# Kernel optimization log

Measured on AMD Instinct MI355X. Metric: run time of the kernel, lower is better.

## Reference

```python
import jax, jax.numpy as jnp
import numpy as np
from jax import lax

H = 12  # num_heads

def conv1d_same(x, w, b):
    # x: [B, Cin, L], w: [Cout, Cin, K] (torch Conv1d layout), 'same' padding
    y = lax.conv_general_dilated(x, w, window_strides=(1,), padding='SAME',
                                 dimension_numbers=('NCH', 'OIH', 'NCH'))
    return y + b[None, :, None]

def setup_inputs() -> dict:
    key = jax.random.key(0)
    ks = jax.random.split(key, 16)
    B, N, C = 8, 4096, 768
    d = C // H
    s = 0.02
    return {
        'x': jax.random.normal(ks[0], (B, N, C), dtype=jnp.float32),
        'qkv_w': jax.random.normal(ks[1], (3 * C, C), dtype=jnp.float32) * s,
        'proj_w': jax.random.normal(ks[2], (C, C), dtype=jnp.float32) * s,
        'proj_b': jnp.zeros((C,), dtype=jnp.float32),
        'conv_w': jax.random.normal(ks[3], (d, d, 5), dtype=jnp.float32) * s,  # k=5 from log2(768)
        'conv_b': jnp.zeros((d,), dtype=jnp.float32),
        'fc_w': jax.random.normal(ks[4], (d, d), dtype=jnp.float32) * s,
        'fc_b': jnp.zeros((d,), dtype=jnp.float32),
        'dw1_w': jax.random.normal(ks[5], (d, d, 3), dtype=jnp.float32) * s,
        'dw1_b': jnp.zeros((d,), dtype=jnp.float32),
        'dw2_w': jax.random.normal(ks[6], (d, d, 5), dtype=jnp.float32) * s,
        'dw2_b': jnp.zeros((d,), dtype=jnp.float32),
    }

def reference(x, qkv_w, proj_w, proj_b, conv_w, conv_b, fc_w, fc_b, dw1_w, dw1_b, dw2_w, dw2_b):
    B, N, C = x.shape
    d = C // H
    scale = d ** (-0.5)
    # qkv projection -> [3, B, H, N, d]
    qkv = (x @ qkv_w.T).reshape(B, N, 3, H, d).transpose(2, 0, 3, 1, 4)
    q, k, v = qkv[0], qkv[1], qkv[2]
    # SE-style gate: global avg over tokens, conv over channel axis, sigmoid
    res = jnp.mean(v, axis=2).reshape(B * H, d, 1)          # [BH, d, 1]
    res = conv1d_same(res, conv_w, conv_b)                   # [BH, d, 1]
    res = jax.nn.sigmoid(res).transpose(0, 2, 1).reshape(B, H, 1, d)
    # value branch: two 1D convs over token axis (channels = head_dim)
    vch = v.reshape(B * H, N, d).transpose(0, 2, 1)          # [BH, d, N]
    v2 = conv1d_same(vch, dw1_w, dw1_b) + conv1d_same(vch, dw2_w, dw2_b)
    v2 = v2.transpose(0, 2, 1).reshape(B, H, N, d)
    # channel attention: (scaled k)^T @ q -> [B, H, d, d]
    kq = jnp.einsum('bhnd,bhne->bhde', k * scale, q)
    a = jax.nn.relu(kq) @ fc_w.T + fc_b
    a = jax.nn.softmax(a + kq, axis=-1)
    # (a @ v2^T)^T -> [B, H, N, d]
    out = jnp.einsum('bhde,bhne->bhnd', a, v2)
    out = res * out
    out = out.transpose(0, 2, 1, 3).reshape(B, N, C)
    return out @ proj_w.T + proj_b
```

## Files before the change

kernel.cpp:

```cpp
#include <hip/hip_runtime.h>
#include <hip/hip_bf16.h>
#include <cstdint>
#include <cstddef>

typedef unsigned short u16;
typedef __attribute__((ext_vector_type(4))) unsigned short u16x4;
typedef __attribute__((ext_vector_type(8))) unsigned short u16x8;
typedef __attribute__((ext_vector_type(8))) short bf16x8;
typedef __attribute__((ext_vector_type(4))) float f32x4;

#define BB 8
#define NN 4096
#define CC 768
#define HH 12
#define DD 64
#define NHEADS 96
#define QKVSZ 25165824LL

__device__ inline float b2f(u16 u) { return __uint_as_float(((unsigned)u) << 16); }
__device__ inline u16 f2b(float f) {
    unsigned u = __float_as_uint(f);
    return (u16)((u + 0x7fffu + ((u >> 16) & 1u)) >> 16);
}
__device__ inline f32x4 zero4() { f32x4 z = {0.f, 0.f, 0.f, 0.f}; return z; }

__device__ __forceinline__ void gl_lds16(const u16* g, u16* l) {
    __builtin_amdgcn_global_load_lds(
        (const __attribute__((address_space(1))) void*)g,
        (__attribute__((address_space(3))) void*)l, 16, 0, 0);
}

__global__ void cast_all(const float* __restrict__ x, const float* __restrict__ w1,
                         const float* __restrict__ w2, u16* __restrict__ xb,
                         u16* __restrict__ wqkv, u16* __restrict__ wproj) {
    const long n0 = 25165824, n1 = 1769472, n2 = 589824;
    long i0 = (long)(blockIdx.x * blockDim.x + threadIdx.x) * 4;
    long stride = (long)gridDim.x * blockDim.x * 4;
    for (long j = i0; j < n0 + n1 + n2; j += stride) {
        const float* s; u16* d; long k;
        if (j < n0)            { s = x;  d = xb;    k = j; }
        else if (j < n0 + n1)  { s = w1; d = wqkv;  k = j - n0; }
        else                   { s = w2; d = wproj; k = j - n0 - n1; }
        float4 v = *(const float4*)(s + k);
        u16x4 o;
        o[0] = f2b(v.x); o[1] = f2b(v.y); o[2] = f2b(v.z); o[3] = f2b(v.w);
        *(u16x4*)(d + k) = o;
    }
}

template <int MODE>
__global__ __launch_bounds__(256) void gemm128e(const u16* __restrict__ A, const u16* __restrict__ Bm,
                                                const float* __restrict__ bias, void* __restrict__ out,
                                                int ncol) {
    constexpr int K = 768;
    constexpr int NT = K / 32;
    __shared__ __align__(16) u16 lA[2][128 * 32];
    __shared__ __align__(16) u16 lB[2][128 * 32];
    const int tid = threadIdx.x;
    const int lane = tid & 63, wid = tid >> 6;
    const int wr = wid >> 1, wc = wid & 1;
    const int li = lane & 15, g = lane >> 4;

    const int nwg = gridDim.x, chunk = nwg >> 3;
    const int swz = ((int)blockIdx.x & 7) * chunk + ((int)blockIdx.x >> 3);
    const int col0 = (swz % ncol) * 128;
    const int row0 = (swz / ncol) * 128;

    const int srow = lane >> 2;
    const int scol = ((lane & 3) ^ ((lane >> 3) & 3)) * 8;

    f32x4 acc[4][4];
#pragma unroll
    for (int i = 0; i < 4; ++i)
#pragma unroll
        for (int j = 0; j < 4; ++j) acc[i][j] = zero4();

    const int r0s = wid * 32;

    gl_lds16(A  + (size_t)(row0 + r0s +      srow) * K + scol, &lA[0][ r0s       * 32]);
    gl_lds16(A  + (size_t)(row0 + r0s + 16 + srow) * K + scol, &lA[0][(r0s + 16) * 32]);
    gl_lds16(Bm + (size_t)(col0 + r0s +      srow) * K + scol, &lB[0][ r0s       * 32]);
    gl_lds16(Bm + (size_t)(col0 + r0s + 16 + srow) * K + scol, &lB[0][(r0s + 16) * 32]);

    int buf = 0;
    for (int t = 0; t < NT; ++t) {
        __syncthreads();
        if (t + 1 < NT) {
            const int kt = (t + 1) * 32;
            const int nb = buf ^ 1;
            gl_lds16(A  + (size_t)(row0 + r0s +      srow) * K + kt + scol, &lA[nb][ r0s       * 32]);
            gl_lds16(A  + (size_t)(row0 + r0s + 16 + srow) * K + kt + scol, &lA[nb][(r0s + 16) * 32]);
            gl_lds16(Bm + (size_t)(col0 + r0s +      srow) * K + kt + scol, &lB[nb][ r0s       * 32]);
            gl_lds16(Bm + (size_t)(col0 + r0s + 16 + srow) * K + kt + scol, &lB[nb][(r0s + 16) * 32]);
        }
        bf16x8 af[4], bf_[4];
#pragma unroll
        for (int i = 0; i < 4; ++i) {
            int ra = wr * 64 + i * 16 + li;
            af[i] = *(const bf16x8*)((const char*)&lA[buf][0] +
                                     ra * 64 + ((g ^ ((ra >> 1) & 3)) << 4));
            int rb = wc * 64 + i * 16 + li;
            bf_[i] = *(const bf16x8*)((const char*)&lB[buf][0] +
                                      rb * 64 + ((g ^ ((rb >> 1) & 3)) << 4));
        }
#pragma unroll
        for (int i = 0; i < 4; ++i)
#pragma unroll
            for (int j = 0; j < 4; ++j)
                acc[i][j] = __builtin_amdgcn_mfma_f32_16x16x32_bf16(af[i], bf_[j], acc[i][j], 0, 0, 0);
        buf ^= 1;
    }

#pragma unroll
    for (int i = 0; i < 4; ++i) {
#pragma unroll
        for (int j = 0; j < 4; ++j) {
            int c = col0 + wc * 64 + j * 16 + li;
            if constexpr (MODE == 0) {
                int part = c / 768, rem = c % 768;
                int h = rem >> 6, dd = rem & 63;
#pragma unroll
                for (int e = 0; e < 4; ++e) {
                    int r = row0 + wr * 64 + i * 16 + g * 4 + e;
                    int b = r >> 12, n = r & 4095;
                    ((u16*)out)[(((size_t)part * NHEADS + b * HH + h) * NN + n) * DD + dd] =
                        f2b(acc[i][j][e]);
                }
            } else {
                float bb = bias[c];
#pragma unroll
                for (int e = 0; e < 4; ++e) {
                    int r = row0 + wr * 64 + i * 16 + g * 4 + e;
                    ((float*)out)[(size_t)r * 768 + c] = acc[i][j][e] + bb;
                }
            }
        }
    }
}

__global__ __launch_bounds__(256) void kq_mean(const u16* __restrict__ qkv, float* __restrict__ kqp,
                                               float* __restrict__ meanp) {
    const int head = blockIdx.x, part = blockIdx.y;
    const int tid = threadIdx.x, lane = tid & 63, wid = tid >> 6;
    __shared__ __align__(16) u16 tiles[4][2][32 * 64];
    __shared__ float sred[16 * 64];

    if (part == 4) {
        const u16* vh = qkv + 2 * QKVSZ + (size_t)head * NN * DD;
        int rg = tid >> 4, cg = tid & 15;
        float s0 = 0.f, s1 = 0.f, s2 = 0.f, s3 = 0.f;
        for (int it = 0; it < 256; ++it) {
            int n = rg + it * 16;
            u16x4 v = *(const u16x4*)(vh + (size_t)n * DD + cg * 4);
            s0 += b2f(v[0]); s1 += b2f(v[1]); s2 += b2f(v[2]); s3 += b2f(v[3]);
        }
        sred[rg * 64 + cg * 4 + 0] = s0;
        sred[rg * 64 + cg * 4 + 1] = s1;
        sred[rg * 64 + cg * 4 + 2] = s2;
        sred[rg * 64 + cg * 4 + 3] = s3;
        __syncthreads();
        if (tid < 64) {
            float s = 0.f;
#pragma unroll
            for (int rg2 = 0; rg2 < 16; ++rg2) s += sred[rg2 * 64 + tid];
            meanp[head * 64 + tid] = s;
        }
        return;
    }

    u16* kt = tiles[wid][0];
    u16* qt = tiles[wid][1];
    const u16* qh = qkv + (size_t)head * NN * DD;
    const u16* kh = qkv + QKVSZ + (size_t)head * NN * DD;
    const int nbase = part * 1024 + wid * 256;

    f32x4 acc[4][4];
#pragma unroll
    for (int i = 0; i < 4; ++i)
#pragma unroll
        for (int j = 0; j < 4; ++j) acc[i][j] = zero4();

    const int srow = lane >> 3, schunk = (lane & 7) * 8;
    const int g8 = (lane >> 4) * 8, li = lane & 15;

    for (int it = 0; it < 8; ++it) {
        int n0 = nbase + it * 32;
#pragma unroll
        for (int p = 0; p < 4; ++p) {
            int r = srow + p * 8;
            *(u16x8*)(kt + r * 64 + schunk) = *(const u16x8*)(kh + (size_t)(n0 + r) * DD + schunk);
            *(u16x8*)(qt + r * 64 + schunk) = *(const u16x8*)(qh + (size_t)(n0 + r) * DD + schunk);
        }
        bf16x8 af[4], bf_[4];
#pragma unroll
        for (int i = 0; i < 4; ++i)
#pragma unroll
            for (int j = 0; j < 8; ++j) af[i][j] = (short)kt[(g8 + j) * 64 + i * 16 + li];
#pragma unroll
        for (int i = 0; i < 4; ++i)
#pragma unroll
            for (int j = 0; j < 8; ++j) bf_[i][j] = (short)qt[(g8 + j) * 64 + i * 16 + li];
#pragma unroll
        for (int i = 0; i < 4; ++i)
#pragma unroll
            for (int j = 0; j < 4; ++j)
                acc[i][j] = __builtin_amdgcn_mfma_f32_16x16x32_bf16(af[i], bf_[j], acc[i][j], 0, 0, 0);
    }

    const int slot = part * 4 + wid;
    const int g = lane >> 4;
    float* dst = kqp + ((size_t)head * 16 + slot) * 4096;
#pragma unroll
    for (int i = 0; i < 4; ++i)
#pragma unroll
        for (int j = 0; j < 4; ++j)
#pragma unroll
            for (int e = 0; e < 4; ++e)
                dst[(i * 16 + g * 4 + e) * 64 + j * 16 + li] = acc[i][j][e];
}

__global__ __launch_bounds__(256) void head_finish(
    const float* __restrict__ kqp, const float* __restrict__ meanp,
    const float* __restrict__ conv_w, const float* __restrict__ conv_b,
    const float* __restrict__ fc_w, const float* __restrict__ fc_b,
    const float* __restrict__ dw1_w, const float* __restrict__ dw1_b,
    const float* __restrict__ dw2_w, const float* __restrict__ dw2_b,
    u16* __restrict__ eff, float* __restrict__ effb) {
    const int head = blockIdx.x;
    const int tid = threadIdx.x;
    __shared__ float skq[64 * 64];
    __shared__ float sa[64 * 64];
    __shared__ float sgate[64];
    __shared__ float sw2[64 * 16 * 5];
    __shared__ float sw1[64 * 16 * 3];

    for (int idx = tid; idx < 4096; idx += 256) {
        float s = 0.f;
#pragma unroll
        for (int p = 0; p < 16; ++p) s += kqp[((size_t)head * 16 + p) * 4096 + idx];
        skq[idx] = s * 0.125f;
    }
    __syncthreads();
    if (tid < 64) {
        float gsum = conv_b[tid];
        for (int i = 0; i < 64; ++i)
            gsum += conv_w[(tid * 64 + i) * 5 + 2] * (meanp[head * 64 + i] * (1.f / 4096.f));
        sgate[tid] = 1.f / (1.f + __expf(-gsum));
    }

    {
        int rr = tid >> 2, cg = (tid & 3) * 16;
        for (int c = cg; c < cg + 16; ++c) {
            float s = fc_b[c];
            for (int e = 0; e < 64; ++e) s += fmaxf(skq[rr * 64 + e], 0.f) * fc_w[c * 64 + e];
            sa[rr * 64 + c] = s + skq[rr * 64 + c];
        }
    }
    __syncthreads();
    if (tid < 64) {
        float m = -1e30f;
        for (int e = 0; e < 64; ++e) m = fmaxf(m, sa[tid * 64 + e]);
        float s = 0.f;
        for (int e = 0; e < 64; ++e) {
            float p = __expf(sa[tid * 64 + e] - m);
            sa[tid * 64 + e] = p;
            s += p;
        }
        float inv = 1.f / s;
        for (int e = 0; e < 64; ++e) sa[tid * 64 + e] *= inv;
    }
    __syncthreads();
    if (tid < 64) {
        float s = 0.f;
        for (int e = 0; e < 64; ++e) s += sa[tid * 64 + e] * (dw1_b[e] + dw2_b[e]);
        effb[head * 64 + tid] = sgate[tid] * s;
    }

    for (int ig = 0; ig < 4; ++ig) {
        __syncthreads();
        for (int idx = tid; idx < 64 * 16 * 5; idx += 256) {
            int e = idx / 80, rem = idx % 80, il2 = rem / 5, t = rem % 5;
            sw2[idx] = dw2_w[((size_t)(e * 64 + ig * 16 + il2)) * 5 + t];
        }
        for (int idx = tid; idx < 64 * 16 * 3; idx += 256) {
            int e = idx / 48, rem = idx % 48, il2 = rem / 3, t = rem % 3;
            sw1[idx] = dw1_w[((size_t)(e * 64 + ig * 16 + il2)) * 3 + t];
        }
        __syncthreads();

        const int il = tid & 15, og = tid >> 4;
        const int i = ig * 16 + il;
        float t[4][5];
#pragma unroll
        for (int o = 0; o < 4; ++o)
#pragma unroll
            for (int tp = 0; tp < 5; ++tp) t[o][tp] = 0.f;

        for (int e = 0; e < 64; ++e) {
            float a0 = sa[(og * 4 + 0) * 64 + e];
            float a1 = sa[(og * 4 + 1) * 64 + e];
            float a2 = sa[(og * 4 + 2) * 64 + e];
            float a3 = sa[(og * 4 + 3) * 64 + e];
            const float* w2 = sw2 + (e * 16 + il) * 5;
            const float* w1 = sw1 + (e * 16 + il) * 3;
            float c0 = w2[0], c1 = w2[1] + w1[0], c2 = w2[2] + w1[1], c3 = w2[3] + w1[2], c4 = w2[4];
            t[0][0] += a0 * c0; t[0][1] += a0 * c1; t[0][2] += a0 * c2; t[0][3] += a0 * c3; t[0][4] += a0 * c4;
            t[1][0] += a1 * c0; t[1][1] += a1 * c1; t[1][2] += a1 * c2; t[1][3] += a1 * c3; t[1][4] += a1 * c4;
            t[2][0] += a2 * c0; t[2][1] += a2 * c1; t[2][2] += a2 * c2; t[2][3] += a2 * c3; t[2][4] += a2 * c4;
            t[3][0] += a3 * c0; t[3][1] += a3 * c1; t[3][2] += a3 * c2; t[3][3] += a3 * c3; t[3][4] += a3 * c4;
        }
#pragma unroll
        for (int o = 0; o < 4; ++o) {
            int oo = og * 4 + o;
            float gt = sgate[oo];
            u16* eo = eff + ((size_t)head * 64 + oo) * 320 + i;
#pragma unroll
            for (int tp = 0; tp < 5; ++tp) eo[tp * 64] = f2b(gt * t[o][tp]);
        }
    }
}

__global__ __launch_bounds__(256) void conv_attn(const u16* __restrict__ qkv, const u16* __restrict__ eff,
                                                 const float* __restrict__ effb, u16* __restrict__ attn) {
    const int nt = blockIdx.x, head = blockIdx.y;
    const int tid = threadIdx.x, lane = tid & 63, wid = tid >> 6;
    __shared__ __align__(16) u16 vt[132 * 64];
    const int n0 = nt * 128;
    const u16* vh = qkv + 2 * QKVSZ + (size_t)head * NN * DD;

    {
        int sr = tid >> 3, sc = (tid & 7) * 8;
#pragma unroll
        for (int p = 0; p < 5; ++p) {
            int r = sr + p * 32;
            if (r < 132) {
                int n = n0 - 2 + r;
                u16x8 v = {0, 0, 0, 0, 0, 0, 0, 0};
                if (n >= 0 && n < NN) v = *(const u16x8*)(vh + (size_t)n * DD + sc);
                *(u16x8*)((char*)vt + ((r * 128 + sc * 2) ^ ((r & 7) << 4))) = v;
            }
        }
    }
    __syncthreads();

    f32x4 acc[2][4];
#pragma unroll
    for (int s = 0; s < 2; ++s)
#pragma unroll
        for (int j = 0; j < 4; ++j) acc[s][j] = zero4();

    const u16* effh = eff + (size_t)head * 64 * 320;
    const int li = lane & 15, g = lane >> 4;
#pragma unroll
    for (int s = 0; s < 10; ++s) {
        int tap = s >> 1, half = s & 1;
        bf16x8 bfr[4];
#pragma unroll
        for (int nj = 0; nj < 4; ++nj)
            bfr[nj] = *(const bf16x8*)(effh + (size_t)(nj * 16 + li) * 320 + s * 32 + g * 8);
        int kc = half * 64 + g * 16;
#pragma unroll
        for (int sub = 0; sub < 2; ++sub) {
            int rr = wid * 32 + sub * 16 + li + tap;
            bf16x8 afr = *(const bf16x8*)((char*)vt + ((rr * 128 + kc) ^ ((rr & 7) << 4)));
#pragma unroll
            for (int nj = 0; nj < 4; ++nj)
                acc[sub][nj] = __builtin_amdgcn_mfma_f32_16x16x32_bf16(afr, bfr[nj], acc[sub][nj], 0, 0, 0);
        }
    }

    const int b = head / HH, h = head % HH;
#pragma unroll
    for (int sub = 0; sub < 2; ++sub)
#pragma unroll
        for (int nj = 0; nj < 4; ++nj) {
            int o = nj * 16 + li;
            float bb = effb[head * 64 + o];
#pragma unroll
            for (int e = 0; e < 4; ++e) {
                int m = wid * 32 + sub * 16 + g * 4 + e;
                size_t n = (size_t)n0 + m;
                attn[((size_t)b * NN + n) * CC + h * DD + o] = f2b(acc[sub][nj][e] + bb);
            }
        }
}

extern "C" void kernel_launch(void* const* d_in, const int* in_sizes, int n_in,
                              void* d_out, int out_size, void* d_ws, size_t ws_size,
                              hipStream_t stream) {
    const float* x      = (const float*)d_in[0];
    const float* qkv_w  = (const float*)d_in[1];
    const float* proj_w = (const float*)d_in[2];
    const float* proj_b = (const float*)d_in[3];
    const float* conv_w = (const float*)d_in[4];
    const float* conv_b = (const float*)d_in[5];
    const float* fc_w   = (const float*)d_in[6];
    const float* fc_b   = (const float*)d_in[7];
    const float* dw1_w  = (const float*)d_in[8];
    const float* dw1_b  = (const float*)d_in[9];
    const float* dw2_w  = (const float*)d_in[10];
    const float* dw2_b  = (const float*)d_in[11];

    char* ws = (char*)d_ws;
    u16* xb    = (u16*)(ws);
    u16* wqkv  = (u16*)(ws + 50331648);
    u16* wproj = (u16*)(ws + 53870592);
    u16* qkv   = (u16*)(ws + 55050240);
    u16* eff   = (u16*)(ws + 206045184);
    float* effb = (float*)(ws + 209977344);
    u16* attn  = (u16*)(ws + 210001920);

    float* kqp   = (float*)(ws);
    float* meanp = (float*)(ws + 25165824);

    float* out = (float*)d_out;

    cast_all<<<2048, 256, 0, stream>>>(x, qkv_w, proj_w, xb, wqkv, wproj);

    gemm128e<0><<<4608, 256, 0, stream>>>(xb, wqkv, nullptr, qkv, 18);

    kq_mean<<<dim3(96, 5), 256, 0, stream>>>(qkv, kqp, meanp);
    head_finish<<<96, 256, 0, stream>>>(kqp, meanp, conv_w, conv_b, fc_w, fc_b,
                                        dw1_w, dw1_b, dw2_w, dw2_b, eff, effb);

    conv_attn<<<dim3(32, 96), 256, 0, stream>>>(qkv, eff, effb, attn);

    gemm128e<1><<<1536, 256, 0, stream>>>(attn, wproj, proj_b, out, 6);
}
```

Baseline: 460.2 us.

## Enlarge GEMM tiles to 256x256 with 512 threads and explicit vmcnt pipelining

Replaces the 128x128x32 GEMM with a 256x256x64 tiled kernel using 8 waves, XOR-swizzled LDS and 8x4 MFMA accumulators per wave. It overlaps global-to-LDS prefetch with compute through explicit s_waitcnt vmcnt and raw barriers, and raises MFMA issue priority with s_setprio. The larger tiles increase operand reuse and reduce global traffic for both the QKV and output projections. In exchange the kernel needs 128KB of LDS and more registers, which lowers occupancy. The proj GEMM drops to 384 blocks, which may leave the GPU under-filled.

Measured after the change: 438.4 us. 4.7% less time.

```diff
diff --git a/kernel.cpp b/kernel.cpp
--- a/kernel.cpp
+++ b/kernel.cpp
@@ -49,70 +49,82 @@
 }
 
 template <int MODE>
-__global__ __launch_bounds__(256) void gemm128e(const u16* __restrict__ A, const u16* __restrict__ Bm,
-                                                const float* __restrict__ bias, void* __restrict__ out,
-                                                int ncol) {
+__global__ __launch_bounds__(512, 2) void gemm256(const u16* __restrict__ A, const u16* __restrict__ Bm,
+                                                  const float* __restrict__ bias, void* __restrict__ out,
+                                                  int ncol) {
     constexpr int K = 768;
-    constexpr int NT = K / 32;
-    __shared__ __align__(16) u16 lA[2][128 * 32];
-    __shared__ __align__(16) u16 lB[2][128 * 32];
+    constexpr int NT = K / 64;
+    __shared__ __align__(16) u16 lA[2][256 * 64];
+    __shared__ __align__(16) u16 lB[2][256 * 64];
     const int tid = threadIdx.x;
     const int lane = tid & 63, wid = tid >> 6;
-    const int wr = wid >> 1, wc = wid & 1;
+    const int wr = wid >> 2, wc = wid & 3;
     const int li = lane & 15, g = lane >> 4;
 
     const int nwg = gridDim.x, chunk = nwg >> 3;
     const int swz = ((int)blockIdx.x & 7) * chunk + ((int)blockIdx.x >> 3);
-    const int col0 = (swz % ncol) * 128;
-    const int row0 = (swz / ncol) * 128;
-
-    const int srow = lane >> 2;
-    const int scol = ((lane & 3) ^ ((lane >> 3) & 3)) * 8;
-
-    f32x4 acc[4][4];
-#pragma unroll
-    for (int i = 0; i < 4; ++i)
+    const int col0 = (swz % ncol) * 256;
+    const int row0 = (swz / ncol) * 256;
+
+    const int lrow = lane >> 3;
+    const int lcolsw = ((lane & 7) ^ lrow) * 8;
+    const int r0s = wid * 32;
+
+    f32x4 acc[8][4];
+#pragma unroll
+    for (int i = 0; i < 8; ++i)
 #pragma unroll
         for (int j = 0; j < 4; ++j) acc[i][j] = zero4();
 
-    const int r0s = wid * 32;
-
-    gl_lds16(A  + (size_t)(row0 + r0s +      srow) * K + scol, &lA[0][ r0s       * 32]);
-    gl_lds16(A  + (size_t)(row0 + r0s + 16 + srow) * K + scol, &lA[0][(r0s + 16) * 32]);
-    gl_lds16(Bm + (size_t)(col0 + r0s +      srow) * K + scol, &lB[0][ r0s       * 32]);
-    gl_lds16(Bm + (size_t)(col0 + r0s + 16 + srow) * K + scol, &lB[0][(r0s + 16) * 32]);
-
-    int buf = 0;
+#pragma unroll
+    for (int s = 0; s < 4; ++s) {
+        int r = r0s + s * 8;
+        gl_lds16(A  + (size_t)(row0 + r + lrow) * K + lcolsw, &lA[0][r * 64]);
+        gl_lds16(Bm + (size_t)(col0 + r + lrow) * K + lcolsw, &lB[0][r * 64]);
+    }
+
     for (int t = 0; t < NT; ++t) {
-        __syncthreads();
+        const int buf = t & 1;
         if (t + 1 < NT) {
-            const int kt = (t + 1) * 32;
-            const int nb = buf ^ 1;
-            gl_lds16(A  + (size_t)(row0 + r0s +      srow) * K + kt + scol, &lA[nb][ r0s       * 32]);
-            gl_lds16(A  + (size_t)(row0 + r0s + 16 + srow) * K + kt + scol, &lA[nb][(r0s + 16) * 32]);
-            gl_lds16(Bm + (size_t)(col0 + r0s +      srow) * K + kt + scol, &lB[nb][ r0s       * 32]);
-            gl_lds16(Bm + (size_t)(col0 + r0s + 16 + srow) * K + kt + scol, &lB[nb][(r0s + 16) * 32]);
-        }
-        bf16x8 af[4], bf_[4];
-#pragma unroll
-        for (int i = 0; i < 4; ++i) {
-            int ra = wr * 64 + i * 16 + li;
-            af[i] = *(const bf16x8*)((const char*)&lA[buf][0] +
-                                     ra * 64 + ((g ^ ((ra >> 1) & 3)) << 4));
-            int rb = wc * 64 + i * 16 + li;
-            bf_[i] = *(const bf16x8*)((const char*)&lB[buf][0] +
-                                      rb * 64 + ((g ^ ((rb >> 1) & 3)) << 4));
-        }
-#pragma unroll
-        for (int i = 0; i < 4; ++i)
-#pragma unroll
-            for (int j = 0; j < 4; ++j)
-                acc[i][j] = __builtin_amdgcn_mfma_f32_16x16x32_bf16(af[i], bf_[j], acc[i][j], 0, 0, 0);
-        buf ^= 1;
-    }
-
-#pragma unroll
-    for (int i = 0; i < 4; ++i) {
+            const int kt = (t + 1) * 64, nb = buf ^ 1;
+#pragma unroll
+            for (int s = 0; s < 4; ++s) {
+                int r = r0s + s * 8;
+                gl_lds16(A  + (size_t)(row0 + r + lrow) * K + kt + lcolsw, &lA[nb][r * 64]);
+                gl_lds16(Bm + (size_t)(col0 + r + lrow) * K + kt + lcolsw, &lB[nb][r * 64]);
+            }
+            asm volatile("s_waitcnt vmcnt(8)" ::: "memory");
+        } else {
+            asm volatile("s_waitcnt vmcnt(0)" ::: "memory");
+        }
+        __builtin_amdgcn_s_barrier();
+
+#pragma unroll
+        for (int ks = 0; ks < 2; ++ks) {
+            bf16x8 bf_[4];
+#pragma unroll
+            for (int j = 0; j < 4; ++j) {
+                int rb = wc * 64 + j * 16 + li;
+                bf_[j] = *(const bf16x8*)((const char*)&lB[buf][0] +
+                                          ((rb * 128 + ks * 64 + g * 16) ^ ((rb & 7) << 4)));
+            }
+            __builtin_amdgcn_s_setprio(1);
+#pragma unroll
+            for (int i = 0; i < 8; ++i) {
+                int ra = wr * 128 + i * 16 + li;
+                bf16x8 af = *(const bf16x8*)((const char*)&lA[buf][0] +
+                                             ((ra * 128 + ks * 64 + g * 16) ^ ((ra & 7) << 4)));
+#pragma unroll
+                for (int j = 0; j < 4; ++j)
+                    acc[i][j] = __builtin_amdgcn_mfma_f32_16x16x32_bf16(af, bf_[j], acc[i][j], 0, 0, 0);
+            }
+            __builtin_amdgcn_s_setprio(0);
+        }
+        __builtin_amdgcn_s_barrier();
+    }
+
+#pragma unroll
+    for (int i = 0; i < 8; ++i) {
 #pragma unroll
         for (int j = 0; j < 4; ++j) {
             int c = col0 + wc * 64 + j * 16 + li;
@@ -121,7 +133,7 @@
                 int h = rem >> 6, dd = rem & 63;
 #pragma unroll
                 for (int e = 0; e < 4; ++e) {
-                    int r = row0 + wr * 64 + i * 16 + g * 4 + e;
+                    int r = row0 + wr * 128 + i * 16 + g * 4 + e;
                     int b = r >> 12, n = r & 4095;
                     ((u16*)out)[(((size_t)part * NHEADS + b * HH + h) * NN + n) * DD + dd] =
                         f2b(acc[i][j][e]);
@@ -130,7 +142,7 @@
                 float bb = bias[c];
 #pragma unroll
                 for (int e = 0; e < 4; ++e) {
-                    int r = row0 + wr * 64 + i * 16 + g * 4 + e;
+                    int r = row0 + wr * 128 + i * 16 + g * 4 + e;
                     ((float*)out)[(size_t)r * 768 + c] = acc[i][j][e] + bb;
                 }
             }
@@ -417,7 +429,7 @@
 
     cast_all<<<2048, 256, 0, stream>>>(x, qkv_w, proj_w, xb, wqkv, wproj);
 
-    gemm128e<0><<<4608, 256, 0, stream>>>(xb, wqkv, nullptr, qkv, 18);
+    gemm256<0><<<1152, 512, 0, stream>>>(xb, wqkv, nullptr, qkv, 9);
 
     kq_mean<<<dim3(96, 5), 256, 0, stream>>>(qkv, kqp, meanp);
     head_finish<<<96, 256, 0, stream>>>(kqp, meanp, conv_w, conv_b, fc_w, fc_b,
@@ -425,5 +437,5 @@
 
     conv_attn<<<dim3(32, 96), 256, 0, stream>>>(qkv, eff, effb, attn);
 
-    gemm128e<1><<<1536, 256, 0, stream>>>(attn, wproj, proj_b, out, 6);
-}
+    gemm256<1><<<384, 512, 0, stream>>>(attn, wproj, proj_b, out, 3);
+}
```
